# Kernel tuning notes

Hardware: AMD Instinct MI355X
Metric: run time of the kernel (lower is better)

## Reference

```python
import jax, jax.numpy as jnp
import numpy as np

TOP_K = 2
N_EXPERTS = 8


def setup_inputs() -> dict:
    key = jax.random.key(0)
    k1, k2, k3 = jax.random.split(key, 3)
    B, S, D, O, E = 2, 4096, 1024, 1024, N_EXPERTS
    scale_in = 1.0 / np.sqrt(D)
    return {
        "x": jax.random.normal(k1, (B, S, D), dtype=jnp.float32),
        "gate_w": jax.random.normal(k2, (E, D), dtype=jnp.float32) * scale_in,
        "gate_b": jnp.zeros((E,), dtype=jnp.float32),
        "expert_w": jax.random.normal(k3, (E, O, D), dtype=jnp.float32) * scale_in,
        "expert_b": jnp.zeros((E, O), dtype=jnp.float32),
    }


def reference(x, gate_w, gate_b, expert_w, expert_b):
    B, S, D = x.shape
    E, O, _ = expert_w.shape
    h = x.reshape(-1, D)  # [T, D] flattened tokens

    # Router: logits -> float32 softmax -> top-k -> renormalized weights
    router_logits = h @ gate_w.T + gate_b  # [T, E]
    probs = jax.nn.softmax(router_logits.astype(jnp.float32), axis=-1)
    topk_w, topk_idx = jax.lax.top_k(probs, TOP_K)  # [T, K]
    topk_w = topk_w / jnp.sum(topk_w, axis=-1, keepdims=True)
    topk_w = topk_w.astype(h.dtype)

    # Dense combine weights per (token, expert): zero for unselected experts.
    combine = jnp.sum(
        jax.nn.one_hot(topk_idx, E, dtype=h.dtype) * topk_w[..., None], axis=1
    )  # [T, E]

    # All-expert outputs, then weighted combine (math-equivalent to
    # per-expert gather-GEMM-scatter since combine is 0 off the top-k).
    expert_out = jnp.einsum("td,eod->teo", h, expert_w) + expert_b[None]  # [T, E, O]
    out = jnp.einsum("te,teo->to", combine, expert_out)  # [T, O]

    return out.reshape(B, S, O), router_logits
```

## Files before the change

### kernel.cpp

```cpp
#include <hip/hip_runtime.h>
#include <hip/hip_bf16.h>
#include <stdint.h>

typedef __attribute__((ext_vector_type(8))) short bf16x8;
typedef __attribute__((ext_vector_type(4))) float f32x4;

#define T_TOKENS 8192
#define DIM 1024
#define NEXP 8
#define NPAIR 28
#define BUFSZ 40960

__device__ __forceinline__ unsigned short f2bf(float f) {
  unsigned u = __float_as_uint(f);
  u = (u + 0x7FFFu + ((u >> 16) & 1u)) >> 16;
  return (unsigned short)u;
}

__global__ __launch_bounds__(256) void router_kernel(
    const float* __restrict__ x, const float* __restrict__ gw, const float* __restrict__ gb,
    float* __restrict__ logits_out, unsigned short* __restrict__ xw,
    int* __restrict__ tk_e, float* __restrict__ tk_w) {
  int wave = threadIdx.x >> 6, lane = threadIdx.x & 63;
  int t = blockIdx.x * 4 + wave;
  float acc[NEXP];
#pragma unroll
  for (int e = 0; e < NEXP; ++e) acc[e] = 0.f;
  const float4* xr = (const float4*)(x + (size_t)t * DIM);
  float4 xv4[4];
#pragma unroll
  for (int it = 0; it < 4; ++it) {
    int d4 = it * 64 + lane;
    float4 xv = xr[d4];
    xv4[it] = xv;
#pragma unroll
    for (int e = 0; e < NEXP; ++e) {
      float4 gv = ((const float4*)(gw + e * DIM))[d4];
      acc[e] += xv.x * gv.x + xv.y * gv.y + xv.z * gv.z + xv.w * gv.w;
    }
  }
#pragma unroll
  for (int off = 32; off; off >>= 1)
#pragma unroll
    for (int e = 0; e < NEXP; ++e) acc[e] += __shfl_xor(acc[e], off);
  float4 gb0 = ((const float4*)gb)[0];
  float4 gb1 = ((const float4*)gb)[1];
  acc[0] += gb0.x; acc[1] += gb0.y; acc[2] += gb0.z; acc[3] += gb0.w;
  acc[4] += gb1.x; acc[5] += gb1.y; acc[6] += gb1.z; acc[7] += gb1.w;
  int e0 = 0; float l0 = acc[0];
#pragma unroll
  for (int e = 1; e < NEXP; ++e) if (acc[e] > l0) { l0 = acc[e]; e0 = e; }
  int e1 = -1; float l1 = -1e30f;
#pragma unroll
  for (int e = 0; e < NEXP; ++e) if (e != e0 && acc[e] > l1) { l1 = acc[e]; e1 = e; }
  float r = expf(l1 - l0);
  float w0 = 1.f / (1.f + r);
  float w1 = r * w0;
  if (lane == 0) {
    float4* lp = (float4*)(logits_out + (size_t)t * NEXP);
    lp[0] = make_float4(acc[0], acc[1], acc[2], acc[3]);
    lp[1] = make_float4(acc[4], acc[5], acc[6], acc[7]);
    tk_e[t * 2] = e0; tk_e[t * 2 + 1] = e1;
    tk_w[t * 2] = w0; tk_w[t * 2 + 1] = w1;
  }
  ushort4* xo0 = (ushort4*)(xw + (size_t)(t * 2) * DIM);
  ushort4* xo1 = (ushort4*)(xw + (size_t)(t * 2 + 1) * DIM);
#pragma unroll
  for (int it = 0; it < 4; ++it) {
    int d4 = it * 64 + lane;
    float4 v = xv4[it];
    ushort4 o0, o1;
    o0.x = f2bf(w0 * v.x); o0.y = f2bf(w0 * v.y); o0.z = f2bf(w0 * v.z); o0.w = f2bf(w0 * v.w);
    o1.x = f2bf(w1 * v.x); o1.y = f2bf(w1 * v.y); o1.z = f2bf(w1 * v.z); o1.w = f2bf(w1 * v.w);
    xo0[d4] = o0;
    xo1[d4] = o1;
  }
}

__global__ __launch_bounds__(1024) void sortconv_kernel(
    const float* __restrict__ ew, unsigned short* __restrict__ w_bf,
    const int* __restrict__ tk_e, const float* __restrict__ tk_w,
    int* __restrict__ offsets_g, int* __restrict__ row_tok2,
    float2* __restrict__ row_wab, int* __restrict__ pairAB_g,
    int* __restrict__ tiles_g, int* __restrict__ n_tiles_g) {
  if (blockIdx.x > 0) {
    int i = (blockIdx.x - 1) * 1024 + threadIdx.x;
    float4 v = ((const float4*)ew)[i];
    ushort4 o;
    o.x = f2bf(v.x); o.y = f2bf(v.y); o.z = f2bf(v.z); o.w = f2bf(v.w);
    ((ushort4*)w_bf)[i] = o;
    return;
  }
  int tid = threadIdx.x;
  int lane = tid & 63, wv = tid >> 6;
  __shared__ unsigned short excl16[NPAIR][1024];
  __shared__ int wavebase[16][NPAIR];
  __shared__ int offs_l[NPAIR + 1];

  int pp[8];
  int rt2[8];
  float wa_[8], wb_[8];
  const int base = tid * 8;
#pragma unroll
  for (int i = 0; i < 8; ++i) {
    int2 ev = ((const int2*)tk_e)[base + i];
    float2 wv2 = ((const float2*)tk_w)[base + i];
    int a, b, ka;
    float wa, wb;
    if (ev.x < ev.y) { a = ev.x; b = ev.y; ka = 0; wa = wv2.x; wb = wv2.y; }
    else             { a = ev.y; b = ev.x; ka = 1; wa = wv2.y; wb = wv2.x; }
    pp[i] = a * (15 - a) / 2 + (b - a - 1);
    rt2[i] = (base + i) * 2 + ka;
    wa_[i] = wa; wb_[i] = wb;
  }

#pragma unroll
  for (int p = 0; p < NPAIR; ++p) {
    int cnt = 0;
#pragma unroll
    for (int i = 0; i < 8; ++i) cnt += (pp[i] == p);
    int incl = cnt;
#pragma unroll
    for (int off = 1; off < 64; off <<= 1) {
      int n = __shfl_up(incl, off);
      if (lane >= off) incl += n;
    }
    excl16[p][tid] = (unsigned short)(incl - cnt);
    if (lane == 63) wavebase[wv][p] = incl;
  }
  __syncthreads();

  if (tid == 0) {
    int tot[NPAIR];
#pragma unroll
    for (int p = 0; p < NPAIR; ++p) tot[p] = 0;
    for (int w = 0; w < 16; ++w)
#pragma unroll
      for (int p = 0; p < NPAIR; ++p) {
        int v = wavebase[w][p];
        wavebase[w][p] = tot[p];
        tot[p] += v;
      }
    int o = 0;
#pragma unroll
    for (int p = 0; p < NPAIR; ++p) { offs_l[p] = o; o += tot[p]; }
    offs_l[NPAIR] = o;
    for (int p = 0; p <= NPAIR; ++p) offsets_g[p] = offs_l[p];
    int pid = 0;
    for (int a = 0; a < 7; ++a)
      for (int b = a + 1; b < 8; ++b) pairAB_g[pid++] = a | (b << 4);
    int nb = 0;
    for (int p = 0; p < NPAIR; ++p) {
      int mt = (tot[p] + 127) >> 7;
      for (int n = 0; n < 2; ++n)
        for (int m = 0; m < mt; ++m) tiles_g[nb++] = p | (n << 5) | (m << 6);
    }
    n_tiles_g[0] = nb;
    n_tiles_g[1] = (nb + 7) >> 3;
  }
  __syncthreads();

#pragma unroll
  for (int i = 0; i < 8; ++i) {
    int p = pp[i];
    int rank = 0;
#pragma unroll
    for (int j = 0; j < 8; ++j)
      if (j < i) rank += (pp[j] == p);
    int pos = offs_l[p] + wavebase[wv][p] + (int)excl16[p][tid] + rank;
    row_tok2[pos] = rt2[i];
    row_wab[pos] = make_float2(wa_[i], wb_[i]);
  }
}

#define GLOAD16(g, l)                                                                   \
  __builtin_amdgcn_global_load_lds((const __attribute__((address_space(1))) unsigned int*)(g), \
                                   (__attribute__((address_space(3))) unsigned int*)(l), 16, 0, 0)

__global__ __launch_bounds__(512, 2) void gemm_kernel(
    const unsigned short* __restrict__ xw, const unsigned short* __restrict__ w_bf,
    const int* __restrict__ row_tok2, const float2* __restrict__ row_wab,
    const int* __restrict__ offsets, const int* __restrict__ pairAB,
    const int* __restrict__ tiles, const int* __restrict__ n_tiles,
    const float* __restrict__ eb, float* __restrict__ out) {
  const int nb = n_tiles[0], cpx = n_tiles[1];
  const int wg = blockIdx.x;
  const int slot = wg >> 3;
  if (slot >= cpx) return;
  const int idx = (wg & 7) * cpx + slot;
  if (idx >= nb) return;
  const int s = tiles[idx];
  const int pid = s & 31;
  const int n0 = ((s >> 5) & 1) << 9;
  const int m0 = (s >> 6) << 7;
  const int ab = pairAB[pid];
  const int ea = ab & 15, ebx = ab >> 4;
  const int seg0 = offsets[pid], segN = offsets[pid + 1] - seg0;

  const int tid = threadIdx.x;
  const int lane = tid & 63, wave = tid >> 6;
  const int wr = wave >> 2, wc = wave & 3;

  __shared__ __align__(16) char smem[3 * BUFSZ];

  const int arow = tid >> 2;
  const int swzc = ((tid & 3) ^ ((tid >> 3) & 3)) << 4;
  const int dA = tid * 16;
  const int dB = 8192 + tid * 16;

  int gr0 = m0 + arow; if (gr0 > segN - 1) gr0 = segN - 1;
  const int idxa = row_tok2[seg0 + gr0];
  const char* srcAa = (const char*)xw + (size_t)idxa * 2048 + swzc;
  const char* srcAb = (const char*)xw + (size_t)(idxa ^ 1) * 2048 + swzc;
  const char* srcBa = (const char*)w_bf + (((size_t)ea << 20) + (size_t)(n0 + arow) * 1024) * 2 + swzc;
  const char* srcBb = (const char*)w_bf + (((size_t)ebx << 20) + (size_t)(n0 + arow) * 1024) * 2 + swzc;

  const int rsw = (((lane >> 4) ^ (lane >> 1)) & 3) << 4;
  int aoff[4], boff[8];
#pragma unroll
  for (int m = 0; m < 4; ++m)
    aoff[m] = (wr * 64 + m * 16 + (lane & 15)) * 64 + rsw;
#pragma unroll
  for (int n = 0; n < 8; ++n)
    boff[n] = 8192 + (wc * 128 + n * 16 + (lane & 15)) * 64 + rsw;

  f32x4 acc[4][8];
#pragma unroll
  for (int m = 0; m < 4; ++m)
#pragma unroll
    for (int n = 0; n < 8; ++n) acc[m][n] = (f32x4){0.f, 0.f, 0.f, 0.f};

#define STAGE5(bufo, pa, pb)                                   \
  {                                                            \
    GLOAD16((pa), smem + (bufo) + dA);                         \
    GLOAD16((pb), smem + (bufo) + dB);                         \
    GLOAD16((pb) + 262144, smem + (bufo) + dB + 8192);         \
    GLOAD16((pb) + 524288, smem + (bufo) + dB + 16384);        \
    GLOAD16((pb) + 786432, smem + (bufo) + dB + 24576);        \
  }
#define STAGEJ(bufo, j)                                                  \
  {                                                                      \
    if ((j) < 32) { const int kb = (j) * 64;                             \
      STAGE5(bufo, srcAa + kb, srcBa + kb); }                            \
    else { const int kb = ((j) - 32) * 64;                               \
      STAGE5(bufo, srcAb + kb, srcBb + kb); }                            \
  }

  STAGEJ(0, 0);
  STAGEJ(BUFSZ, 1);

  int cb = 0;
  for (int kt = 0; kt < 64; ++kt) {
    if (kt < 63) {
      asm volatile("s_waitcnt vmcnt(5)" ::: "memory");
    } else {
      asm volatile("s_waitcnt vmcnt(0)" ::: "memory");
    }
    __builtin_amdgcn_s_barrier();
    const int cur = cb * BUFSZ;
    bf16x8 a_[4], b_[8];
#pragma unroll
    for (int m = 0; m < 4; ++m) a_[m] = *(const bf16x8*)(smem + cur + aoff[m]);
#pragma unroll
    for (int n = 0; n < 8; ++n) b_[n] = *(const bf16x8*)(smem + cur + boff[n]);
    if (kt < 62) {
      int cbn = cb + 2; if (cbn >= 3) cbn -= 3;
      STAGEJ(cbn * BUFSZ, kt + 2);
    }
    __builtin_amdgcn_s_setprio(1);
#pragma unroll
    for (int m = 0; m < 4; ++m)
#pragma unroll
      for (int n = 0; n < 8; ++n)
        acc[m][n] = __builtin_amdgcn_mfma_f32_16x16x32_bf16(a_[m], b_[n], acc[m][n], 0, 0, 0);
    __builtin_amdgcn_s_setprio(0);
    cb = (cb + 1 == 3) ? 0 : cb + 1;
  }

  const float* ba = eb + ea * 1024;
  const float* bb = eb + ebx * 1024;
#pragma unroll
  for (int m = 0; m < 4; ++m) {
#pragma unroll
    for (int r = 0; r < 4; ++r) {
      int g = m0 + wr * 64 + m * 16 + ((lane >> 4) << 2) + r;
      if (g < segN) {
        int p = seg0 + g;
        float2 wab = row_wab[p];
        int token = row_tok2[p] >> 1;
        float* op = out + (size_t)token * 1024;
#pragma unroll
        for (int n = 0; n < 8; ++n) {
          int col = n0 + wc * 128 + n * 16 + (lane & 15);
          op[col] = acc[m][n][r] + wab.x * ba[col] + wab.y * bb[col];
        }
      }
    }
  }
#undef STAGEJ
#undef STAGE5
}

extern "C" void kernel_launch(void* const* d_in, const int* in_sizes, int n_in,
                              void* d_out, int out_size, void* d_ws, size_t ws_size,
                              hipStream_t stream) {
  const float* x  = (const float*)d_in[0];
  const float* gw = (const float*)d_in[1];
  const float* gb = (const float*)d_in[2];
  const float* ew = (const float*)d_in[3];
  const float* eb = (const float*)d_in[4];
  float* out = (float*)d_out;
  float* logits = out + (size_t)T_TOKENS * 1024;

  char* ws = (char*)d_ws;
  unsigned short* xw   = (unsigned short*)(ws);
  unsigned short* w_bf = (unsigned short*)(ws + 33554432);
  int*    tk_e     = (int*)(ws + 50331648);
  float*  tk_w     = (float*)(ws + 50397184);
  int*    row_tok2 = (int*)(ws + 50462720);
  float2* row_wab  = (float2*)(ws + 50528256);
  int*    offsets  = (int*)(ws + 50593792);
  int*    pairAB   = (int*)(ws + 50593920);
  int*    n_tiles  = (int*)(ws + 50594048);
  int*    tiles    = (int*)(ws + 50594176);

  router_kernel<<<2048, 256, 0, stream>>>(x, gw, gb, logits, xw, tk_e, tk_w);
  sortconv_kernel<<<2049, 1024, 0, stream>>>(ew, w_bf, tk_e, tk_w, offsets, row_tok2,
                                             row_wab, pairAB, tiles, n_tiles);
  gemm_kernel<<<256, 512, 0, stream>>>(xw, w_bf, row_tok2, row_wab, offsets, pairAB,
                                       tiles, n_tiles, eb, out);
}
```

Baseline: 109.6 us.

## Store unscaled bf16 tokens once and apply routing weights by rescaling accumulators

The router now writes a single unscaled bf16 copy of each token instead of two weight-prescaled copies, halving that write traffic and the activation footprint. The GEMM reads the same A row for both experts. At the midpoint of K it scales the accumulator by wa/wb, and at the end by wb, so the result is wa*Xa + wb*Xb. This cuts router store bandwidth and workspace but adds a division and a rescale pass, with a clamp on small wb that can affect precision when one weight is tiny.

```diff
diff --git a/kernel.cpp b/kernel.cpp
--- a/kernel.cpp
+++ b/kernel.cpp
@@ -27,12 +27,14 @@
 #pragma unroll
   for (int e = 0; e < NEXP; ++e) acc[e] = 0.f;
   const float4* xr = (const float4*)(x + (size_t)t * DIM);
-  float4 xv4[4];
+  ushort4* xo = (ushort4*)(xw + (size_t)t * DIM);
 #pragma unroll
   for (int it = 0; it < 4; ++it) {
     int d4 = it * 64 + lane;
     float4 xv = xr[d4];
-    xv4[it] = xv;
+    ushort4 xb;
+    xb.x = f2bf(xv.x); xb.y = f2bf(xv.y); xb.z = f2bf(xv.z); xb.w = f2bf(xv.w);
+    xo[d4] = xb;
 #pragma unroll
     for (int e = 0; e < NEXP; ++e) {
       float4 gv = ((const float4*)(gw + e * DIM))[d4];
@@ -43,44 +45,32 @@
   for (int off = 32; off; off >>= 1)
 #pragma unroll
     for (int e = 0; e < NEXP; ++e) acc[e] += __shfl_xor(acc[e], off);
-  float4 gb0 = ((const float4*)gb)[0];
-  float4 gb1 = ((const float4*)gb)[1];
-  acc[0] += gb0.x; acc[1] += gb0.y; acc[2] += gb0.z; acc[3] += gb0.w;
-  acc[4] += gb1.x; acc[5] += gb1.y; acc[6] += gb1.z; acc[7] += gb1.w;
-  int e0 = 0; float l0 = acc[0];
-#pragma unroll
-  for (int e = 1; e < NEXP; ++e) if (acc[e] > l0) { l0 = acc[e]; e0 = e; }
-  int e1 = -1; float l1 = -1e30f;
-#pragma unroll
-  for (int e = 0; e < NEXP; ++e) if (e != e0 && acc[e] > l1) { l1 = acc[e]; e1 = e; }
-  float r = expf(l1 - l0);
-  float w0 = 1.f / (1.f + r);
-  float w1 = r * w0;
   if (lane == 0) {
+    float4 gb0 = ((const float4*)gb)[0];
+    float4 gb1 = ((const float4*)gb)[1];
+    acc[0] += gb0.x; acc[1] += gb0.y; acc[2] += gb0.z; acc[3] += gb0.w;
+    acc[4] += gb1.x; acc[5] += gb1.y; acc[6] += gb1.z; acc[7] += gb1.w;
     float4* lp = (float4*)(logits_out + (size_t)t * NEXP);
     lp[0] = make_float4(acc[0], acc[1], acc[2], acc[3]);
     lp[1] = make_float4(acc[4], acc[5], acc[6], acc[7]);
+    int e0 = 0; float l0 = acc[0];
+#pragma unroll
+    for (int e = 1; e < NEXP; ++e) if (acc[e] > l0) { l0 = acc[e]; e0 = e; }
+    int e1 = -1; float l1 = -1e30f;
+#pragma unroll
+    for (int e = 0; e < NEXP; ++e) if (e != e0 && acc[e] > l1) { l1 = acc[e]; e1 = e; }
+    float r = expf(l1 - l0);
+    float w0 = 1.f / (1.f + r);
+    float w1 = r * w0;
     tk_e[t * 2] = e0; tk_e[t * 2 + 1] = e1;
     tk_w[t * 2] = w0; tk_w[t * 2 + 1] = w1;
-  }
-  ushort4* xo0 = (ushort4*)(xw + (size_t)(t * 2) * DIM);
-  ushort4* xo1 = (ushort4*)(xw + (size_t)(t * 2 + 1) * DIM);
-#pragma unroll
-  for (int it = 0; it < 4; ++it) {
-    int d4 = it * 64 + lane;
-    float4 v = xv4[it];
-    ushort4 o0, o1;
-    o0.x = f2bf(w0 * v.x); o0.y = f2bf(w0 * v.y); o0.z = f2bf(w0 * v.z); o0.w = f2bf(w0 * v.w);
-    o1.x = f2bf(w1 * v.x); o1.y = f2bf(w1 * v.y); o1.z = f2bf(w1 * v.z); o1.w = f2bf(w1 * v.w);
-    xo0[d4] = o0;
-    xo1[d4] = o1;
   }
 }
 
 __global__ __launch_bounds__(1024) void sortconv_kernel(
     const float* __restrict__ ew, unsigned short* __restrict__ w_bf,
     const int* __restrict__ tk_e, const float* __restrict__ tk_w,
-    int* __restrict__ offsets_g, int* __restrict__ row_tok2,
+    int* __restrict__ offsets_g, int* __restrict__ row_tok,
     float2* __restrict__ row_wab, int* __restrict__ pairAB_g,
     int* __restrict__ tiles_g, int* __restrict__ n_tiles_g) {
   if (blockIdx.x > 0) {
@@ -98,19 +88,17 @@
   __shared__ int offs_l[NPAIR + 1];
 
   int pp[8];
-  int rt2[8];
   float wa_[8], wb_[8];
   const int base = tid * 8;
 #pragma unroll
   for (int i = 0; i < 8; ++i) {
     int2 ev = ((const int2*)tk_e)[base + i];
     float2 wv2 = ((const float2*)tk_w)[base + i];
-    int a, b, ka;
+    int a, b;
     float wa, wb;
-    if (ev.x < ev.y) { a = ev.x; b = ev.y; ka = 0; wa = wv2.x; wb = wv2.y; }
-    else             { a = ev.y; b = ev.x; ka = 1; wa = wv2.y; wb = wv2.x; }
+    if (ev.x < ev.y) { a = ev.x; b = ev.y; wa = wv2.x; wb = wv2.y; }
+    else             { a = ev.y; b = ev.x; wa = wv2.y; wb = wv2.x; }
     pp[i] = a * (15 - a) / 2 + (b - a - 1);
-    rt2[i] = (base + i) * 2 + ka;
     wa_[i] = wa; wb_[i] = wb;
   }
 
@@ -168,7 +156,7 @@
     for (int j = 0; j < 8; ++j)
       if (j < i) rank += (pp[j] == p);
     int pos = offs_l[p] + wavebase[wv][p] + (int)excl16[p][tid] + rank;
-    row_tok2[pos] = rt2[i];
+    row_tok[pos] = base + i;
     row_wab[pos] = make_float2(wa_[i], wb_[i]);
   }
 }
@@ -179,7 +167,7 @@
 
 __global__ __launch_bounds__(512, 2) void gemm_kernel(
     const unsigned short* __restrict__ xw, const unsigned short* __restrict__ w_bf,
-    const int* __restrict__ row_tok2, const float2* __restrict__ row_wab,
+    const int* __restrict__ row_tok, const float2* __restrict__ row_wab,
     const int* __restrict__ offsets, const int* __restrict__ pairAB,
     const int* __restrict__ tiles, const int* __restrict__ n_tiles,
     const float* __restrict__ eb, float* __restrict__ out) {
@@ -209,11 +197,24 @@
   const int dB = 8192 + tid * 16;
 
   int gr0 = m0 + arow; if (gr0 > segN - 1) gr0 = segN - 1;
-  const int idxa = row_tok2[seg0 + gr0];
-  const char* srcAa = (const char*)xw + (size_t)idxa * 2048 + swzc;
-  const char* srcAb = (const char*)xw + (size_t)(idxa ^ 1) * 2048 + swzc;
+  const char* srcA = (const char*)xw + (size_t)row_tok[seg0 + gr0] * 2048 + swzc;
   const char* srcBa = (const char*)w_bf + (((size_t)ea << 20) + (size_t)(n0 + arow) * 1024) * 2 + swzc;
   const char* srcBb = (const char*)w_bf + (((size_t)ebx << 20) + (size_t)(n0 + arow) * 1024) * 2 + swzc;
+
+  float rat[4][4], wav[4][4], wbe[4][4];
+#pragma unroll
+  for (int m = 0; m < 4; ++m) {
+#pragma unroll
+    for (int r = 0; r < 4; ++r) {
+      int g = m0 + wr * 64 + m * 16 + ((lane >> 4) << 2) + r;
+      if (g > segN - 1) g = segN - 1;
+      float2 wab = row_wab[seg0 + g];
+      float we = fmaxf(wab.y, 1e-20f);
+      wav[m][r] = wab.x;
+      wbe[m][r] = we;
+      rat[m][r] = wab.x / we;
+    }
+  }
 
   const int rsw = (((lane >> 4) ^ (lane >> 1)) & 3) << 4;
   int aoff[4], boff[8];
@@ -241,9 +242,9 @@
 #define STAGEJ(bufo, j)                                                  \
   {                                                                      \
     if ((j) < 32) { const int kb = (j) * 64;                             \
-      STAGE5(bufo, srcAa + kb, srcBa + kb); }                            \
+      STAGE5(bufo, srcA + kb, srcBa + kb); }                             \
     else { const int kb = ((j) - 32) * 64;                               \
-      STAGE5(bufo, srcAb + kb, srcBb + kb); }                            \
+      STAGE5(bufo, srcA + kb, srcBb + kb); }                             \
   }
 
   STAGEJ(0, 0);
@@ -267,6 +268,14 @@
       int cbn = cb + 2; if (cbn >= 3) cbn -= 3;
       STAGEJ(cbn * BUFSZ, kt + 2);
     }
+    if (kt == 32) {
+#pragma unroll
+      for (int m = 0; m < 4; ++m)
+#pragma unroll
+        for (int n = 0; n < 8; ++n)
+#pragma unroll
+          for (int r = 0; r < 4; ++r) acc[m][n][r] *= rat[m][r];
+    }
     __builtin_amdgcn_s_setprio(1);
 #pragma unroll
     for (int m = 0; m < 4; ++m)
@@ -286,13 +295,13 @@
       int g = m0 + wr * 64 + m * 16 + ((lane >> 4) << 2) + r;
       if (g < segN) {
         int p = seg0 + g;
-        float2 wab = row_wab[p];
-        int token = row_tok2[p] >> 1;
+        float wa = wav[m][r], we = wbe[m][r];
+        int token = row_tok[p];
         float* op = out + (size_t)token * 1024;
 #pragma unroll
         for (int n = 0; n < 8; ++n) {
           int col = n0 + wc * 128 + n * 16 + (lane & 15);
-          op[col] = acc[m][n][r] + wab.x * ba[col] + wab.y * bb[col];
+          op[col] = we * acc[m][n][r] + wa * ba[col] + we * bb[col];
         }
       }
     }
@@ -314,19 +323,19 @@
 
   char* ws = (char*)d_ws;
   unsigned short* xw   = (unsigned short*)(ws);
-  unsigned short* w_bf = (unsigned short*)(ws + 33554432);
-  int*    tk_e     = (int*)(ws + 50331648);
-  float*  tk_w     = (float*)(ws + 50397184);
-  int*    row_tok2 = (int*)(ws + 50462720);
-  float2* row_wab  = (float2*)(ws + 50528256);
-  int*    offsets  = (int*)(ws + 50593792);
-  int*    pairAB   = (int*)(ws + 50593920);
-  int*    n_tiles  = (int*)(ws + 50594048);
-  int*    tiles    = (int*)(ws + 50594176);
+  unsigned short* w_bf = (unsigned short*)(ws + 16777216);
+  int*    tk_e     = (int*)(ws + 33554432);
+  float*  tk_w     = (float*)(ws + 33619968);
+  int*    row_tok  = (int*)(ws + 33685504);
+  float2* row_wab  = (float2*)(ws + 33751040);
+  int*    offsets  = (int*)(ws + 33816576);
+  int*    pairAB   = (int*)(ws + 33816704);
+  int*    n_tiles  = (int*)(ws + 33816832);
+  int*    tiles    = (int*)(ws + 33816960);
 
   router_kernel<<<2048, 256, 0, stream>>>(x, gw, gb, logits, xw, tk_e, tk_w);
-  sortconv_kernel<<<2049, 1024, 0, stream>>>(ew, w_bf, tk_e, tk_w, offsets, row_tok2,
+  sortconv_kernel<<<2049, 1024, 0, stream>>>(ew, w_bf, tk_e, tk_w, offsets, row_tok,
                                              row_wab, pairAB, tiles, n_tiles);
-  gemm_kernel<<<256, 512, 0, stream>>>(xw, w_bf, row_tok2, row_wab, offsets, pairAB,
+  gemm_kernel<<<256, 512, 0, stream>>>(xw, w_bf, row_tok, row_wab, offsets, pairAB,
                                        tiles, n_tiles, eb, out);
 }
```

New measurement: 108.4 us. Within noise of the previous version (-1.1%).
